# Optimization experiments

Measured on AMD Instinct MI355X. Metric: run time of the kernel, lower is better.

The kernel has to match this reference:

```python
import jax, jax.numpy as jnp
import numpy as np

GRID = 16  # int(sqrt(num_patches=256))
# fixed ragged grid shapes: 32 images cycling through 4 aspect ratios
_SHAPES = np.array([[32, 32], [16, 64], [24, 40], [40, 24]] * 8, dtype=np.int64)  # [32,2]
_SIZES = _SHAPES[:, 0] * _SHAPES[:, 1]  # per-image patch counts
_SEQ_LEN = int(_SIZES.sum())  # 31744


def setup_inputs() -> dict:
    key = jax.random.key(0)
    k1, k2, k3 = jax.random.split(key, 3)
    return {
        "seq_patches": jax.random.normal(k1, (_SEQ_LEN, 768), dtype=jnp.float32),
        "w": jax.random.normal(k2, (1152, 768), dtype=jnp.float32) * 0.02,
        "b": jnp.zeros((1152,), dtype=jnp.float32),
        "pos_emb": jax.random.normal(k3, (256, 1152), dtype=jnp.float32) * 0.02,
        "seq_sizes": jnp.asarray(_SIZES),
        "spatial_shapes": jnp.asarray(_SHAPES),
    }


def reference(seq_patches, w, b, pos_emb, seq_sizes, spatial_shapes):
    # Linear patch embedding: [S, 768] @ [768, 1152] + [1152]
    patch_embeds = seq_patches @ w.T + b
    d = pos_emb.shape[-1]
    pos_grid = pos_emb.reshape(GRID, GRID, d)  # [16,16,D]
    shapes = np.asarray(spatial_shapes)  # static host-side shapes (ragged loop)
    pos_list = []
    for h, wd in shapes:
        # antialiased bilinear resize, half-pixel centers (align_corners=False)
        rp = jax.image.resize(pos_grid, (int(h), int(wd), d), method="linear", antialias=True)
        pos_list.append(rp.reshape(int(h) * int(wd), d))
    pos_embeds = jnp.concatenate(pos_list, axis=0)  # [S, D]
    return patch_embeds + pos_embeds
```

## Files before the change

kernel.cpp:

```cpp
#include <hip/hip_runtime.h>
#include <hip/hip_bf16.h>
#include <cstdint>
#include <cstddef>

typedef __attribute__((ext_vector_type(8))) short short8;
typedef __attribute__((ext_vector_type(4))) float f32x4;

static constexpr int M_TOT = 31744;
static constexpr int N_TOT = 1152;
static constexpr int K_TOT = 768;
static constexpr long A_ELEMS = (long)M_TOT * K_TOT;
static constexpr long W_ELEMS = (long)N_TOT * K_TOT;
static constexpr int CYC_ROWS = 3968;

__device__ __forceinline__ unsigned short f2bf(float f) {
  unsigned int u = __float_as_uint(f);
  u += 0x7FFFu + ((u >> 16) & 1u);
  return (unsigned short)(u >> 16);
}
__device__ __forceinline__ float bf2f(unsigned short u) {
  return __uint_as_float((unsigned int)u << 16);
}

__global__ void cvt_kernel(const float* __restrict__ A, const float* __restrict__ W,
                           unsigned short* __restrict__ dst) {
  long chunk = (long)blockIdx.x * blockDim.x + threadIdx.x;
  long i = chunk * 8;
  const float* src = (i < A_ELEMS) ? (A + i) : (W + (i - A_ELEMS));
  float4 v0 = *(const float4*)(src);
  float4 v1 = *(const float4*)(src + 4);
  short8 o;
  o[0] = (short)f2bf(v0.x); o[1] = (short)f2bf(v0.y);
  o[2] = (short)f2bf(v0.z); o[3] = (short)f2bf(v0.w);
  o[4] = (short)f2bf(v1.x); o[5] = (short)f2bf(v1.y);
  o[6] = (short)f2bf(v1.z); o[7] = (short)f2bf(v1.w);
  *(short8*)(dst + i) = o;
}

__global__ void tab_kernel(const float* __restrict__ pos, const float* __restrict__ bias,
                           unsigned short* __restrict__ tab) {
  const int t = blockIdx.x * blockDim.x + threadIdx.x;
  const int row = t / 144;
  const int dc = (t - row * 144) * 8;

  int rr, cc; float sy, sx;
  if (row < 1024)      { rr = row >> 5; cc = row & 31; sy = 0.5f;         sx = 0.5f; }
  else if (row < 2048) { const int li = row - 1024; rr = li >> 6; cc = li & 63; sy = 1.0f; sx = 0.25f; }
  else if (row < 3008) { const int li = row - 2048; rr = li / 40; cc = li - rr * 40; sy = 16.0f / 24.0f; sx = 0.4f; }
  else                 { const int li = row - 3008; rr = li / 24; cc = li - rr * 24; sy = 0.4f; sx = 16.0f / 24.0f; }
  float yc = fminf(fmaxf(((float)rr + 0.5f) * sy - 0.5f, 0.0f), 15.0f);
  const int y0 = (int)yc; const float fy = yc - (float)y0;
  const int y1 = y0 < 15 ? y0 + 1 : 15;
  float xc = fminf(fmaxf(((float)cc + 0.5f) * sx - 0.5f, 0.0f), 15.0f);
  const int x0 = (int)xc; const float fx = xc - (float)x0;
  const int x1 = x0 < 15 ? x0 + 1 : 15;
  const float w11 = fy * fx;
  const float w10 = fy - w11;
  const float w01 = fx - w11;
  const float w00 = 1.0f - fy - fx + w11;
  const float* p00 = pos + (size_t)(y0 * 16 + x0) * 1152 + dc;
  const float* p01 = pos + (size_t)(y0 * 16 + x1) * 1152 + dc;
  const float* p10 = pos + (size_t)(y1 * 16 + x0) * 1152 + dc;
  const float* p11 = pos + (size_t)(y1 * 16 + x1) * 1152 + dc;
  const float* bi  = bias + dc;
  short8 o;
#pragma unroll
  for (int j = 0; j < 8; ++j) {
    const float v = bi[j] + w00 * p00[j] + w01 * p01[j] + w10 * p10[j] + w11 * p11[j];
    o[j] = (short)f2bf(v);
  }
  *(short8*)(tab + (size_t)row * 1152 + dc) = o;
}

__device__ __forceinline__ void gload_lds16(const void* g, void* l) {
  __builtin_amdgcn_global_load_lds((__attribute__((address_space(1))) void*)g,
                                   (__attribute__((address_space(3))) void*)l, 16, 0, 0);
}

__global__ __launch_bounds__(256) void gemm_kernel(
    const unsigned short* __restrict__ Abf, const unsigned short* __restrict__ Wbf,
    const unsigned short* __restrict__ tab, float* __restrict__ outp) {
  __shared__ __attribute__((aligned(16))) unsigned short As[2][128 * 64];
  __shared__ __attribute__((aligned(16))) unsigned short Bs[2][128 * 64];

  const int bid = blockIdx.x;
  const int tile = (bid & 7) * 279 + (bid >> 3);
  const int tm = tile / 9, tn = tile % 9;
  const int m0 = tm * 128, n0 = tn * 128;

  const int tid = threadIdx.x;
  const int wid = tid >> 6, lane = tid & 63;
  const int wr = wid >> 1, wc = wid & 1;
  const int rb = wid * 32;
  const int lrow = lane >> 3;
  const int lcol = ((lane & 7) ^ lrow) * 8;
  const int kg = lane >> 4, l15 = lane & 15;

  f32x4 acc[4][4] = {};

  const unsigned short* Abase = Abf + (size_t)m0 * K_TOT;
  const unsigned short* Bbase = Wbf + (size_t)n0 * K_TOT;

#define STAGE(p, kt)                                                             \
  { const int k0_ = (kt) * 64;                                                   \
    _Pragma("unroll") for (int c = 0; c < 4; ++c) {                              \
      const int row_ = rb + c * 8;                                               \
      gload_lds16(Abase + (size_t)(row_ + lrow) * K_TOT + k0_ + lcol,            \
                  (char*)As[p] + row_ * 128);                                    \
      gload_lds16(Bbase + (size_t)(row_ + lrow) * K_TOT + k0_ + lcol,            \
                  (char*)Bs[p] + row_ * 128);                                    \
    } }

#define COMPUTE(p)                                                               \
  { __builtin_amdgcn_s_setprio(1);                                               \
    _Pragma("unroll") for (int kk = 0; kk < 2; ++kk) {                           \
      short8 fa[4], fb[4];                                                       \
      _Pragma("unroll") for (int m = 0; m < 4; ++m) {                            \
        const int arow = wr * 64 + m * 16 + l15;                                 \
        fa[m] = *(const short8*)((const char*)As[p] + arow * 128 +               \
                                 (((kk * 4 + kg) ^ (arow & 7)) << 4));           \
      }                                                                          \
      _Pragma("unroll") for (int n = 0; n < 4; ++n) {                            \
        const int brow = wc * 64 + n * 16 + l15;                                 \
        fb[n] = *(const short8*)((const char*)Bs[p] + brow * 128 +               \
                                 (((kk * 4 + kg) ^ (brow & 7)) << 4));           \
      }                                                                          \
      _Pragma("unroll") for (int m = 0; m < 4; ++m)                              \
        _Pragma("unroll") for (int n = 0; n < 4; ++n)                            \
          acc[m][n] = __builtin_amdgcn_mfma_f32_16x16x32_bf16(                   \
              fa[m], fb[n], acc[m][n], 0, 0, 0);                                 \
    }                                                                            \
    __builtin_amdgcn_s_setprio(0); }

  STAGE(0, 0)
  asm volatile("s_waitcnt vmcnt(0)" ::: "memory");
  __builtin_amdgcn_s_barrier();

#pragma unroll
  for (int t = 0; t < 11; ++t) {
    const int p = t & 1, q = p ^ 1;
    STAGE(q, t + 1)
    COMPUTE(p)
    asm volatile("s_waitcnt vmcnt(0)" ::: "memory");
    __builtin_amdgcn_s_barrier();
  }
  COMPUTE(1)

#undef STAGE
#undef COMPUTE

  const int s_base = m0 + wr * 64 + ((lane >> 4) << 2);
  const int rem_base = s_base % CYC_ROWS;
  const int d_base = n0 + wc * 64 + l15;

#pragma unroll
  for (int m = 0; m < 4; ++m) {
#pragma unroll
    for (int r = 0; r < 4; ++r) {
      const int off = m * 16 + r;
      int rem = rem_base + off;
      if (rem >= CYC_ROWS) rem -= CYC_ROWS;
      const unsigned short* trow = tab + (size_t)rem * 1152 + d_base;
      float* orow = outp + (size_t)(s_base + off) * 1152 + d_base;
#pragma unroll
      for (int n = 0; n < 4; ++n)
        orow[n * 16] = acc[m][n][r] + bf2f(trow[n * 16]);
    }
  }
}

extern "C" void kernel_launch(void* const* d_in, const int* in_sizes, int n_in,
                              void* d_out, int out_size, void* d_ws, size_t ws_size,
                              hipStream_t stream) {
  const float* A    = (const float*)d_in[0];
  const float* W    = (const float*)d_in[1];
  const float* bias = (const float*)d_in[2];
  const float* pos  = (const float*)d_in[3];
  unsigned short* Abf = (unsigned short*)d_ws;
  unsigned short* Wbf = Abf + A_ELEMS;
  unsigned short* tab = Wbf + W_ELEMS;
  float* outp = (float*)d_out;

  cvt_kernel<<<12336, 256, 0, stream>>>(A, W, Abf);
  tab_kernel<<<2232, 256, 0, stream>>>(pos, bias, tab);
  gemm_kernel<<<2232, 256, 0, stream>>>(Abf, Wbf, tab, outp);
}
```

Before: 118.0 us.

## Switch GEMM mainloop to triple-buffered K=32 stages with deeper prefetch

Replaces the double-buffered K=64 LDS pipeline with a three-stage ring of K=32 tiles. Two stages are now in flight, and partial vmcnt waits are used instead of a full drain each iteration. The LDS staging addressing and XOR swizzle are rewritten for 64-byte rows. The aim is to hide global-load latency better, at the cost of two barriers per K-step and half as many MFMAs per barrier.

Result: no change. 117.0 us (-0.9%).

```diff
diff --git a/kernel.cpp b/kernel.cpp
--- a/kernel.cpp
+++ b/kernel.cpp
@@ -80,8 +80,8 @@
 __global__ __launch_bounds__(256) void gemm_kernel(
     const unsigned short* __restrict__ Abf, const unsigned short* __restrict__ Wbf,
     const unsigned short* __restrict__ tab, float* __restrict__ outp) {
-  __shared__ __attribute__((aligned(16))) unsigned short As[2][128 * 64];
-  __shared__ __attribute__((aligned(16))) unsigned short Bs[2][128 * 64];
+  __shared__ __attribute__((aligned(16))) unsigned short As[3][128 * 32];
+  __shared__ __attribute__((aligned(16))) unsigned short Bs[3][128 * 32];
 
   const int bid = blockIdx.x;
   const int tile = (bid & 7) * 279 + (bid >> 3);
@@ -91,60 +91,62 @@
   const int tid = threadIdx.x;
   const int wid = tid >> 6, lane = tid & 63;
   const int wr = wid >> 1, wc = wid & 1;
-  const int rb = wid * 32;
-  const int lrow = lane >> 3;
-  const int lcol = ((lane & 7) ^ lrow) * 8;
   const int kg = lane >> 4, l15 = lane & 15;
+
+  const int srow = lane >> 2;
+  const int schunk = ((lane & 3) ^ ((lane >> 3) & 3)) * 8;
+  const unsigned short* Abase = Abf + (size_t)(m0 + wid * 16 + srow) * K_TOT + schunk;
+  const unsigned short* Bbase = Wbf + (size_t)(n0 + wid * 16 + srow) * K_TOT + schunk;
+  const int wu = wid << 10;
+
+  const int rkey = (l15 >> 1) & 3;
 
   f32x4 acc[4][4] = {};
 
-  const unsigned short* Abase = Abf + (size_t)m0 * K_TOT;
-  const unsigned short* Bbase = Wbf + (size_t)n0 * K_TOT;
-
 #define STAGE(p, kt)                                                             \
-  { const int k0_ = (kt) * 64;                                                   \
-    _Pragma("unroll") for (int c = 0; c < 4; ++c) {                              \
-      const int row_ = rb + c * 8;                                               \
-      gload_lds16(Abase + (size_t)(row_ + lrow) * K_TOT + k0_ + lcol,            \
-                  (char*)As[p] + row_ * 128);                                    \
-      gload_lds16(Bbase + (size_t)(row_ + lrow) * K_TOT + k0_ + lcol,            \
-                  (char*)Bs[p] + row_ * 128);                                    \
-    } }
+  { const int k0_ = (kt) * 32;                                                   \
+    gload_lds16(Abase + k0_,                      (char*)As[p] + wu);            \
+    gload_lds16(Abase + (size_t)64 * K_TOT + k0_, (char*)As[p] + 4096 + wu);     \
+    gload_lds16(Bbase + k0_,                      (char*)Bs[p] + wu);            \
+    gload_lds16(Bbase + (size_t)64 * K_TOT + k0_, (char*)Bs[p] + 4096 + wu); }
 
 #define COMPUTE(p)                                                               \
   { __builtin_amdgcn_s_setprio(1);                                               \
-    _Pragma("unroll") for (int kk = 0; kk < 2; ++kk) {                           \
-      short8 fa[4], fb[4];                                                       \
-      _Pragma("unroll") for (int m = 0; m < 4; ++m) {                            \
-        const int arow = wr * 64 + m * 16 + l15;                                 \
-        fa[m] = *(const short8*)((const char*)As[p] + arow * 128 +               \
-                                 (((kk * 4 + kg) ^ (arow & 7)) << 4));           \
-      }                                                                          \
-      _Pragma("unroll") for (int n = 0; n < 4; ++n) {                            \
-        const int brow = wc * 64 + n * 16 + l15;                                 \
-        fb[n] = *(const short8*)((const char*)Bs[p] + brow * 128 +               \
-                                 (((kk * 4 + kg) ^ (brow & 7)) << 4));           \
-      }                                                                          \
-      _Pragma("unroll") for (int m = 0; m < 4; ++m)                              \
-        _Pragma("unroll") for (int n = 0; n < 4; ++n)                            \
-          acc[m][n] = __builtin_amdgcn_mfma_f32_16x16x32_bf16(                   \
-              fa[m], fb[n], acc[m][n], 0, 0, 0);                                 \
+    short8 fa[4], fb[4];                                                         \
+    _Pragma("unroll") for (int m = 0; m < 4; ++m) {                              \
+      const int arow = wr * 64 + m * 16 + l15;                                   \
+      fa[m] = *(const short8*)((const char*)As[p] + arow * 64 +                  \
+                               ((kg ^ rkey) << 4));                              \
     }                                                                            \
+    _Pragma("unroll") for (int n = 0; n < 4; ++n) {                              \
+      const int brow = wc * 64 + n * 16 + l15;                                   \
+      fb[n] = *(const short8*)((const char*)Bs[p] + brow * 64 +                  \
+                               ((kg ^ rkey) << 4));                              \
+    }                                                                            \
+    _Pragma("unroll") for (int m = 0; m < 4; ++m)                                \
+      _Pragma("unroll") for (int n = 0; n < 4; ++n)                              \
+        acc[m][n] = __builtin_amdgcn_mfma_f32_16x16x32_bf16(                     \
+            fa[m], fb[n], acc[m][n], 0, 0, 0);                                   \
     __builtin_amdgcn_s_setprio(0); }
 
   STAGE(0, 0)
-  asm volatile("s_waitcnt vmcnt(0)" ::: "memory");
-  __builtin_amdgcn_s_barrier();
+  STAGE(1, 1)
 
 #pragma unroll
-  for (int t = 0; t < 11; ++t) {
-    const int p = t & 1, q = p ^ 1;
-    STAGE(q, t + 1)
+  for (int t = 0; t < 24; ++t) {
+    const int p = t % 3;
+    if (t + 2 < 24) {
+      STAGE((t + 2) % 3, t + 2)
+      asm volatile("s_waitcnt vmcnt(8)" ::: "memory");
+    } else if (t + 1 < 24) {
+      asm volatile("s_waitcnt vmcnt(4)" ::: "memory");
+    } else {
+      asm volatile("s_waitcnt vmcnt(0)" ::: "memory");
+    }
+    __builtin_amdgcn_s_barrier();
     COMPUTE(p)
-    asm volatile("s_waitcnt vmcnt(0)" ::: "memory");
     __builtin_amdgcn_s_barrier();
   }
-  COMPUTE(1)
 
 #undef STAGE
 #undef COMPUTE
```

## Fuse fp32-to-bf16 activation conversion into GEMM and load B fragments directly

Applied to the files above, without the earlier changes.

The separate pass that converted the whole activation matrix to bf16 is removed. The GEMM now reads fp32 A from global memory into registers, packs it to bf16 with v_cvt_pk_bf16_f32, and writes it to swizzled LDS. B fragments are loaded straight from global memory into registers instead of going through LDS. The W conversion and the table build are merged into one prep kernel. This avoids writing and re-reading a roughly 48MB bf16 copy and saves a launch, at the cost of fp32 A reads repeated across the 9 N-tiles, register-staged loads with more pressure, and uncoalesced per-lane B reads.

After: 153.9 us. 30.4% more time.

```diff
diff --git a/kernel.cpp b/kernel.cpp
--- a/kernel.cpp
+++ b/kernel.cpp
@@ -9,7 +9,6 @@
 static constexpr int M_TOT = 31744;
 static constexpr int N_TOT = 1152;
 static constexpr int K_TOT = 768;
-static constexpr long A_ELEMS = (long)M_TOT * K_TOT;
 static constexpr long W_ELEMS = (long)N_TOT * K_TOT;
 static constexpr int CYC_ROWS = 3968;
 
@@ -21,25 +20,29 @@
 __device__ __forceinline__ float bf2f(unsigned short u) {
   return __uint_as_float((unsigned int)u << 16);
 }
-
-__global__ void cvt_kernel(const float* __restrict__ A, const float* __restrict__ W,
-                           unsigned short* __restrict__ dst) {
-  long chunk = (long)blockIdx.x * blockDim.x + threadIdx.x;
-  long i = chunk * 8;
-  const float* src = (i < A_ELEMS) ? (A + i) : (W + (i - A_ELEMS));
-  float4 v0 = *(const float4*)(src);
-  float4 v1 = *(const float4*)(src + 4);
-  short8 o;
-  o[0] = (short)f2bf(v0.x); o[1] = (short)f2bf(v0.y);
-  o[2] = (short)f2bf(v0.z); o[3] = (short)f2bf(v0.w);
-  o[4] = (short)f2bf(v1.x); o[5] = (short)f2bf(v1.y);
-  o[6] = (short)f2bf(v1.z); o[7] = (short)f2bf(v1.w);
-  *(short8*)(dst + i) = o;
+__device__ __forceinline__ unsigned int cvtpk(float lo, float hi) {
+  unsigned int r;
+  asm("v_cvt_pk_bf16_f32 %0, %1, %2" : "=v"(r) : "v"(lo), "v"(hi));
+  return r;
 }
 
-__global__ void tab_kernel(const float* __restrict__ pos, const float* __restrict__ bias,
-                           unsigned short* __restrict__ tab) {
-  const int t = blockIdx.x * blockDim.x + threadIdx.x;
+__global__ void prep_kernel(const float* __restrict__ W, const float* __restrict__ pos,
+                            const float* __restrict__ bias,
+                            unsigned short* __restrict__ Wbf, unsigned short* __restrict__ tab) {
+  const int b = blockIdx.x;
+  if (b < 432) {
+    const long i = ((long)b * 256 + threadIdx.x) * 8;
+    float4 v0 = *(const float4*)(W + i);
+    float4 v1 = *(const float4*)(W + i + 4);
+    short8 o;
+    o[0] = (short)f2bf(v0.x); o[1] = (short)f2bf(v0.y);
+    o[2] = (short)f2bf(v0.z); o[3] = (short)f2bf(v0.w);
+    o[4] = (short)f2bf(v1.x); o[5] = (short)f2bf(v1.y);
+    o[6] = (short)f2bf(v1.z); o[7] = (short)f2bf(v1.w);
+    *(short8*)(Wbf + i) = o;
+    return;
+  }
+  const int t = (b - 432) * 256 + threadIdx.x;
   const int row = t / 144;
   const int dc = (t - row * 144) * 8;
 
@@ -72,16 +75,10 @@
   *(short8*)(tab + (size_t)row * 1152 + dc) = o;
 }
 
-__device__ __forceinline__ void gload_lds16(const void* g, void* l) {
-  __builtin_amdgcn_global_load_lds((__attribute__((address_space(1))) void*)g,
-                                   (__attribute__((address_space(3))) void*)l, 16, 0, 0);
-}
-
-__global__ __launch_bounds__(256) void gemm_kernel(
-    const unsigned short* __restrict__ Abf, const unsigned short* __restrict__ Wbf,
+__global__ __launch_bounds__(256, 3) void gemm_kernel(
+    const float* __restrict__ Afp, const unsigned short* __restrict__ Wbf,
     const unsigned short* __restrict__ tab, float* __restrict__ outp) {
   __shared__ __attribute__((aligned(16))) unsigned short As[2][128 * 64];
-  __shared__ __attribute__((aligned(16))) unsigned short Bs[2][128 * 64];
 
   const int bid = blockIdx.x;
   const int tile = (bid & 7) * 279 + (bid >> 3);
@@ -92,61 +89,74 @@
   const int wid = tid >> 6, lane = tid & 63;
   const int wr = wid >> 1, wc = wid & 1;
   const int rb = wid * 32;
-  const int lrow = lane >> 3;
-  const int lcol = ((lane & 7) ^ lrow) * 8;
   const int kg = lane >> 4, l15 = lane & 15;
+  const int dsw = (((lane & 7) ^ (lane >> 3)) << 4);
 
   f32x4 acc[4][4] = {};
+  float4 f0[4], f1[4];
+  short8 fbt[4][2];
 
-  const unsigned short* Abase = Abf + (size_t)m0 * K_TOT;
-  const unsigned short* Bbase = Wbf + (size_t)n0 * K_TOT;
+#define ALOAD(kt)                                                                \
+  _Pragma("unroll") for (int c = 0; c < 4; ++c) {                                \
+    const float* s_ = Afp + (size_t)(m0 + rb + c * 8 + (lane >> 3)) * K_TOT +    \
+                      (kt) * 64 + (lane & 7) * 8;                                \
+    f0[c] = *(const float4*)s_;                                                  \
+    f1[c] = *(const float4*)(s_ + 4);                                            \
+  }
 
-#define STAGE(p, kt)                                                             \
-  { const int k0_ = (kt) * 64;                                                   \
-    _Pragma("unroll") for (int c = 0; c < 4; ++c) {                              \
-      const int row_ = rb + c * 8;                                               \
-      gload_lds16(Abase + (size_t)(row_ + lrow) * K_TOT + k0_ + lcol,            \
-                  (char*)As[p] + row_ * 128);                                    \
-      gload_lds16(Bbase + (size_t)(row_ + lrow) * K_TOT + k0_ + lcol,            \
-                  (char*)Bs[p] + row_ * 128);                                    \
-    } }
+#define AWRITE(q_)                                                               \
+  _Pragma("unroll") for (int c = 0; c < 4; ++c) {                                \
+    int4 w_;                                                                     \
+    w_.x = (int)cvtpk(f0[c].x, f0[c].y);                                         \
+    w_.y = (int)cvtpk(f0[c].z, f0[c].w);                                         \
+    w_.z = (int)cvtpk(f1[c].x, f1[c].y);                                         \
+    w_.w = (int)cvtpk(f1[c].z, f1[c].w);                                         \
+    *(int4*)((char*)As[q_] + (rb + c * 8 + (lane >> 3)) * 128 + dsw) = w_;       \
+  }
 
-#define COMPUTE(p)                                                               \
+#define BLOAD(kt)                                                                \
+  _Pragma("unroll") for (int n = 0; n < 4; ++n) {                                \
+    const unsigned short* s_ = Wbf + (size_t)(n0 + wc * 64 + n * 16 + l15) *     \
+                               K_TOT + (kt) * 64 + kg * 8;                       \
+    fbt[n][0] = *(const short8*)s_;                                              \
+    fbt[n][1] = *(const short8*)(s_ + 32);                                       \
+  }
+
+#define COMPUTE(p_)                                                              \
   { __builtin_amdgcn_s_setprio(1);                                               \
     _Pragma("unroll") for (int kk = 0; kk < 2; ++kk) {                           \
-      short8 fa[4], fb[4];                                                       \
+      short8 fa[4];                                                              \
       _Pragma("unroll") for (int m = 0; m < 4; ++m) {                            \
         const int arow = wr * 64 + m * 16 + l15;                                 \
-        fa[m] = *(const short8*)((const char*)As[p] + arow * 128 +               \
+        fa[m] = *(const short8*)((const char*)As[p_] + arow * 128 +              \
                                  (((kk * 4 + kg) ^ (arow & 7)) << 4));           \
-      }                                                                          \
-      _Pragma("unroll") for (int n = 0; n < 4; ++n) {                            \
-        const int brow = wc * 64 + n * 16 + l15;                                 \
-        fb[n] = *(const short8*)((const char*)Bs[p] + brow * 128 +               \
-                                 (((kk * 4 + kg) ^ (brow & 7)) << 4));           \
       }                                                                          \
       _Pragma("unroll") for (int m = 0; m < 4; ++m)                              \
         _Pragma("unroll") for (int n = 0; n < 4; ++n)                            \
           acc[m][n] = __builtin_amdgcn_mfma_f32_16x16x32_bf16(                   \
-              fa[m], fb[n], acc[m][n], 0, 0, 0);                                 \
+              fa[m], fbt[n][kk], acc[m][n], 0, 0, 0);                            \
     }                                                                            \
     __builtin_amdgcn_s_setprio(0); }
 
-  STAGE(0, 0)
-  asm volatile("s_waitcnt vmcnt(0)" ::: "memory");
-  __builtin_amdgcn_s_barrier();
+  ALOAD(0)
+  AWRITE(0)
+  __syncthreads();
 
 #pragma unroll
-  for (int t = 0; t < 11; ++t) {
-    const int p = t & 1, q = p ^ 1;
-    STAGE(q, t + 1)
-    COMPUTE(p)
-    asm volatile("s_waitcnt vmcnt(0)" ::: "memory");
-    __builtin_amdgcn_s_barrier();
+  for (int t = 0; t < 12; ++t) {
+    if (t < 11) ALOAD(t + 1)
+    BLOAD(t)
+    __builtin_amdgcn_sched_barrier(0);
+    COMPUTE(t & 1)
+    if (t < 11) {
+      AWRITE((t & 1) ^ 1)
+      __syncthreads();
+    }
   }
-  COMPUTE(1)
 
-#undef STAGE
+#undef ALOAD
+#undef AWRITE
+#undef BLOAD
 #undef COMPUTE
 
   const int s_base = m0 + wr * 64 + ((lane >> 4) << 2);
@@ -176,12 +186,10 @@
   const float* W    = (const float*)d_in[1];
   const float* bias = (const float*)d_in[2];
   const float* pos  = (const float*)d_in[3];
-  unsigned short* Abf = (unsigned short*)d_ws;
-  unsigned short* Wbf = Abf + A_ELEMS;
+  unsigned short* Wbf = (unsigned short*)d_ws;
   unsigned short* tab = Wbf + W_ELEMS;
   float* outp = (float*)d_out;
 
-  cvt_kernel<<<12336, 256, 0, stream>>>(A, W, Abf);
-  tab_kernel<<<2232, 256, 0, stream>>>(pos, bias, tab);
-  gemm_kernel<<<2232, 256, 0, stream>>>(Abf, Wbf, tab, outp);
+  prep_kernel<<<2664, 256, 0, stream>>>(W, pos, bias, Wbf, tab);
+  gemm_kernel<<<2232, 256, 0, stream>>>(A, Wbf, tab, outp);
 }
```
